# Performance work log

Hardware: AMD Instinct MI355X
Metric: run time of the kernel (lower is better)

The kernel has to match this reference:

```python
import jax, jax.numpy as jnp
import numpy as np

M, N, D = 100000, 64, 128  # points, channels, voxel grid side


def setup_inputs() -> dict:
    key = jax.random.key(0)
    k1, k2, k3, k4, k5 = jax.random.split(key, 5)
    rng = np.random.default_rng(0)
    # unique occupied voxels in a D^3 grid (Minkowski coords are unique)
    lin = rng.choice(D ** 3, size=M, replace=False)
    coords = np.stack(np.unravel_index(lin, (D, D, D)), axis=1).astype(np.int32)
    w_scale = 0.02  # ~1/sqrt(fan_in=27*N)
    return {
        "feats": jax.random.normal(k1, (M, N), dtype=jnp.float32),
        "W1": jax.random.normal(k2, (27, N, N), dtype=jnp.float32) * w_scale,
        "b1": jax.random.normal(k3, (N,), dtype=jnp.float32) * 0.01,
        "W2": jax.random.normal(k4, (27, N, N), dtype=jnp.float32) * w_scale,
        "b2": jax.random.normal(k5, (N,), dtype=jnp.float32) * 0.01,
        "coords": jnp.asarray(coords),
        "grid_size": D,
    }


def reference(feats, W1, b1, W2, b2, coords, grid_size):
    Dg = grid_size
    m = feats.shape[0]
    # dense hash: linear voxel id -> point index (-1 if empty)
    lin = (coords[:, 0].astype(jnp.int32) * Dg + coords[:, 1]) * Dg + coords[:, 2]
    lookup = jnp.full((Dg * Dg * Dg,), -1, dtype=jnp.int32).at[lin].set(
        jnp.arange(m, dtype=jnp.int32))
    offsets = jnp.array([[i, j, k] for i in (-1, 0, 1) for j in (-1, 0, 1)
                         for k in (-1, 0, 1)], dtype=jnp.int32)  # [27,3]

    def sparse_conv(x, W, b):
        # out[u] = b + sum_k W_k^T gather(x, u+off_k); scan over 27 offsets keeps
        # only one [M,N] gathered buffer live (memory-bound gather-GEMM-scatter)
        def step(acc, wk_off):
            W_k, off = wk_off
            nc = coords + off  # [M,3]
            inb = jnp.all((nc >= 0) & (nc < Dg), axis=1)
            nlin = (nc[:, 0] * Dg + nc[:, 1]) * Dg + nc[:, 2]
            nidx = lookup[jnp.where(inb, nlin, 0)]
            valid = inb & (nidx >= 0)
            g = jnp.where(valid[:, None], x[jnp.maximum(nidx, 0)], 0.0)  # [M,N]
            return acc + g @ W_k, None
        init = jnp.zeros_like(x) + b
        out, _ = jax.lax.scan(step, init, (W, offsets))
        return out

    h = jax.nn.relu(sparse_conv(feats, W1, b1))
    return jax.nn.relu(sparse_conv(h, W2, b2))
```

## Files before the change

### kernel.cpp

```cpp
#include <hip/hip_runtime.h>
#include <hip/hip_bf16.h>
#include <cstdint>
#include <cstddef>

typedef _Float16 half8 __attribute__((ext_vector_type(8)));
typedef float floatx16 __attribute__((ext_vector_type(16)));

#define DGRID 128
#define D3 (DGRID * DGRID * DGRID)
#define WSZ (2 * 27 * 4096)

struct __attribute__((aligned(4))) I3 { int a, b, c; };

__global__ void prep(const int* __restrict__ coords, const float* __restrict__ feats,
                     const float* __restrict__ W1, const float* __restrict__ W2,
                     int* __restrict__ lookup, _Float16* __restrict__ Whf,
                     _Float16* __restrict__ h0, _Float16* __restrict__ h, int M) {
    int tid = blockIdx.x * 256 + threadIdx.x;
    if (tid < WSZ) {
        int idx = tid;
        int j = idx & 7;
        int l = (idx >> 3) & 63;
        int f = (idx >> 9) & 7;
        int kL = idx >> 12;
        int k = kL % 27, L = kL / 27;
        int kk = f & 3, ct = f >> 2;
        int c = kk * 16 + (l >> 5) * 8 + j;
        int n = ct * 32 + (l & 31);
        const float* W = L ? W2 : W1;
        Whf[idx] = (_Float16)W[k * 4096 + c * 64 + n];
        return;
    }
    tid -= WSZ;
    if (tid < M) {
        int x = coords[3 * tid], y = coords[3 * tid + 1], z = coords[3 * tid + 2];
        lookup[(x * DGRID + y) * DGRID + z] = tid;
        return;
    }
    tid -= M;
    if (tid < 64) {
        h0[(size_t)M * 64 + tid] = (_Float16)0.f;
        h[(size_t)M * 64 + tid] = (_Float16)0.f;
        return;
    }
    tid -= 64;
    if (tid < M * 8) {
        const float4* src = (const float4*)feats + (size_t)tid * 2;
        float4 f0 = src[0], f1 = src[1];
        half8 v;
        v[0] = (_Float16)f0.x; v[1] = (_Float16)f0.y;
        v[2] = (_Float16)f0.z; v[3] = (_Float16)f0.w;
        v[4] = (_Float16)f1.x; v[5] = (_Float16)f1.y;
        v[6] = (_Float16)f1.z; v[7] = (_Float16)f1.w;
        ((half8*)h0)[tid] = v;
    }
}

template <bool FIRST, bool OUT_F16>
__global__ __launch_bounds__(64, 1) void spconv(const _Float16* __restrict__ x,
                                                const _Float16* __restrict__ Whf,
                                                const float* __restrict__ bias,
                                                const int* __restrict__ coords,
                                                const int* __restrict__ lookup,
                                                int* __restrict__ nbr,
                                                void* __restrict__ outp, int M) {
    __shared__ int nvs[27 * 128];
    const int lane = threadIdx.x;
    const int lrow = lane & 31;
    const int lhalf = lane >> 5;
    const int mw = blockIdx.x * 128;

#pragma unroll
    for (int half = 0; half < 2; ++half) {
        const int r = half * 64 + lane;
        const int row = mw + r;
        if constexpr (FIRST) {
            if (row < M) {
                int X = coords[3 * row], Y = coords[3 * row + 1], Z = coords[3 * row + 2];
                int zlo = Z - 1;
                if (zlo < 0) zlo = 0;
                if (zlo > DGRID - 3) zlo = DGRID - 3;
                const int zi = Z - zlo;
#pragma unroll
                for (int dx = -1; dx <= 1; ++dx)
#pragma unroll
                    for (int dy = -1; dy <= 1; ++dy) {
                        int nx = X + dx, ny = Y + dy;
                        int v0 = -1, v1 = -1, v2 = -1;
                        if (((unsigned)nx < DGRID) && ((unsigned)ny < DGRID)) {
                            I3 t = *(const I3*)(lookup + ((nx * DGRID + ny) * DGRID + zlo));
                            v0 = t.a; v1 = t.b; v2 = t.c;
                        }
#pragma unroll
                        for (int dz = -1; dz <= 1; ++dz) {
                            int zc = Z + dz;
                            int i = zi + dz;
                            int val = (i == 0) ? v0 : (i == 1) ? v1 : v2;
                            int nidx = M;
                            if (((unsigned)zc < DGRID) && ((unsigned)val < (unsigned)M))
                                nidx = val;
                            int k = (dx + 1) * 9 + (dy + 1) * 3 + (dz + 1);
                            nvs[k * 128 + r] = nidx;
                            nbr[(size_t)k * M + row] = nidx;
                        }
                    }
            } else {
#pragma unroll
                for (int k = 0; k < 27; ++k) nvs[k * 128 + r] = M;
            }
        } else {
            const int rc = row < M ? row : M - 1;
#pragma unroll
            for (int k = 0; k < 27; ++k) nvs[k * 128 + r] = nbr[(size_t)k * M + rc];
        }
    }
    __syncthreads();

    floatx16 acc[8];
#pragma unroll
    for (int i = 0; i < 8; ++i)
#pragma unroll
        for (int j = 0; j < 16; ++j) acc[i][j] = 0.0f;

    const half8* wb = (const half8*)Whf + lane;

    auto loadB = [&](half8* dst, int k) {
#pragma unroll
        for (int f = 0; f < 8; ++f) dst[f] = wb[(k * 8 + f) * 64];
    };
    auto loadA = [&](half8* dst, const int* nv) {
#pragma unroll
        for (int rt = 0; rt < 4; ++rt) {
            const half8* p = (const half8*)(x + (size_t)nv[rt] * 64 + lhalf * 8);
#pragma unroll
            for (int kk = 0; kk < 4; ++kk) dst[rt * 4 + kk] = p[kk * 2];
        }
    };

    int nvr[4][4];
#pragma unroll
    for (int j = 0; j < 3; ++j)
#pragma unroll
        for (int rt = 0; rt < 4; ++rt) nvr[j][rt] = nvs[j * 128 + rt * 32 + lrow];

    half8 Ar[3][16], Br[2][8];
    loadB(Br[0], 0);
    loadA(Ar[0], nvr[0]);
    loadA(Ar[1], nvr[1]);

#pragma unroll
    for (int i = 0; i < 27; ++i) {
        {
            int jn = i + 3;
            if (jn < 27) {
#pragma unroll
                for (int rt = 0; rt < 4; ++rt)
                    nvr[jn & 3][rt] = nvs[jn * 128 + rt * 32 + lrow];
            }
        }
        if (i + 1 < 27) loadB(Br[(i + 1) & 1], i + 1);
        {
            int ja = i + 2;
            if (ja < 27) loadA(Ar[ja % 3], nvr[ja & 3]);
        }
        __builtin_amdgcn_sched_barrier(0);
        half8* A = Ar[i % 3];
        half8* B = Br[i & 1];
#pragma unroll
        for (int kk = 0; kk < 4; ++kk)
#pragma unroll
            for (int rt = 0; rt < 4; ++rt)
#pragma unroll
                for (int ct = 0; ct < 2; ++ct)
                    acc[rt * 2 + ct] = __builtin_amdgcn_mfma_f32_32x32x16_f16(
                        A[rt * 4 + kk], B[ct * 4 + kk], acc[rt * 2 + ct], 0, 0, 0);
    }

    const float bv0 = bias[lrow], bv1 = bias[32 + lrow];
#pragma unroll
    for (int rt = 0; rt < 4; ++rt)
#pragma unroll
        for (int ct = 0; ct < 2; ++ct) {
            const float bb = ct ? bv1 : bv0;
#pragma unroll
            for (int reg = 0; reg < 16; ++reg) {
                int row = (reg & 3) + 8 * (reg >> 2) + 4 * lhalf;
                int g = mw + rt * 32 + row;
                if (g < M) {
                    float v = acc[rt * 2 + ct][reg] + bb;
                    v = v > 0.f ? v : 0.f;
                    size_t off = (size_t)g * 64 + ct * 32 + lrow;
                    if constexpr (OUT_F16)
                        ((_Float16*)outp)[off] = (_Float16)v;
                    else
                        ((float*)outp)[off] = v;
                }
            }
        }
}

extern "C" void kernel_launch(void* const* d_in, const int* in_sizes, int n_in,
                              void* d_out, int out_size, void* d_ws, size_t ws_size,
                              hipStream_t stream) {
    const float* feats = (const float*)d_in[0];
    const float* W1 = (const float*)d_in[1];
    const float* b1 = (const float*)d_in[2];
    const float* W2 = (const float*)d_in[3];
    const float* b2 = (const float*)d_in[4];
    const int* coords = (const int*)d_in[5];
    const int M = in_sizes[0] / 64;

    int* lookup = (int*)d_ws;
    int* nbr = lookup + (size_t)D3;
    _Float16* h = (_Float16*)(nbr + (size_t)27 * M);
    _Float16* h0 = h + (size_t)(M + 1) * 64;
    _Float16* Whf = h0 + (size_t)(M + 1) * 64;
    size_t need = (size_t)D3 * 4 + (size_t)27 * M * 4 +
                  2 * (size_t)(M + 1) * 64 * 2 + (size_t)WSZ * 2;
    if (ws_size < need) return;

    long long pt = (long long)WSZ + M + 64 + (long long)M * 8;
    prep<<<(int)((pt + 255) / 256), 256, 0, stream>>>(coords, feats, W1, W2, lookup, Whf,
                                                      h0, h, M);

    int cb = (M + 127) / 128;
    spconv<true, true><<<cb, 64, 0, stream>>>(h0, Whf, b1, coords, lookup, nbr,
                                              (void*)h, M);
    spconv<false, false><<<cb, 64, 0, stream>>>(h, Whf + (size_t)27 * 4096, b2, coords,
                                                lookup, nbr, d_out, M);
}
```

Before: 175.0 us.

## Split 128-row tile across four waves, one 32-row strip each

Each spconv block now runs 256 threads (four waves) instead of one wave. Each wave computes a 32-row strip of the 128-row tile, so per-thread accumulators and A-operand registers shrink by four. The neighbor-table fill is split across two thread halves. The intent is higher occupancy and more latency hiding for the gather loads. The cost is that every wave loads the full weight slice redundantly, which quadruples weight traffic per block.

After: 196.4 us. 12.2% more time.

```diff
diff --git a/kernel.cpp b/kernel.cpp
--- a/kernel.cpp
+++ b/kernel.cpp
@@ -57,23 +57,26 @@
 }
 
 template <bool FIRST, bool OUT_F16>
-__global__ __launch_bounds__(64, 1) void spconv(const _Float16* __restrict__ x,
-                                                const _Float16* __restrict__ Whf,
-                                                const float* __restrict__ bias,
-                                                const int* __restrict__ coords,
-                                                const int* __restrict__ lookup,
-                                                int* __restrict__ nbr,
-                                                void* __restrict__ outp, int M) {
+__global__ __launch_bounds__(256, 2) void spconv(const _Float16* __restrict__ x,
+                                                 const _Float16* __restrict__ Whf,
+                                                 const float* __restrict__ bias,
+                                                 const int* __restrict__ coords,
+                                                 const int* __restrict__ lookup,
+                                                 int* __restrict__ nbr,
+                                                 void* __restrict__ outp, int M) {
     __shared__ int nvs[27 * 128];
-    const int lane = threadIdx.x;
+    const int tid = threadIdx.x;
+    const int lane = tid & 63;
+    const int wid = tid >> 6;
     const int lrow = lane & 31;
     const int lhalf = lane >> 5;
     const int mw = blockIdx.x * 128;
-
-#pragma unroll
-    for (int half = 0; half < 2; ++half) {
-        const int r = half * 64 + lane;
-        const int row = mw + r;
+    const int wr = wid * 32;
+
+    {
+        const int rr = tid & 127;
+        const int kh = tid >> 7;
+        const int row = mw + rr;
         if constexpr (FIRST) {
             if (row < M) {
                 int X = coords[3 * row], Y = coords[3 * row + 1], Z = coords[3 * row + 2];
@@ -81,44 +84,46 @@
                 if (zlo < 0) zlo = 0;
                 if (zlo > DGRID - 3) zlo = DGRID - 3;
                 const int zi = Z - zlo;
-#pragma unroll
-                for (int dx = -1; dx <= 1; ++dx)
-#pragma unroll
-                    for (int dy = -1; dy <= 1; ++dy) {
-                        int nx = X + dx, ny = Y + dy;
-                        int v0 = -1, v1 = -1, v2 = -1;
-                        if (((unsigned)nx < DGRID) && ((unsigned)ny < DGRID)) {
-                            I3 t = *(const I3*)(lookup + ((nx * DGRID + ny) * DGRID + zlo));
-                            v0 = t.a; v1 = t.b; v2 = t.c;
-                        }
-#pragma unroll
-                        for (int dz = -1; dz <= 1; ++dz) {
-                            int zc = Z + dz;
-                            int i = zi + dz;
-                            int val = (i == 0) ? v0 : (i == 1) ? v1 : v2;
-                            int nidx = M;
-                            if (((unsigned)zc < DGRID) && ((unsigned)val < (unsigned)M))
-                                nidx = val;
-                            int k = (dx + 1) * 9 + (dy + 1) * 3 + (dz + 1);
-                            nvs[k * 128 + r] = nidx;
-                            nbr[(size_t)k * M + row] = nidx;
-                        }
+                const int p0 = kh ? 5 : 0, p1 = kh ? 9 : 5;
+#pragma unroll
+                for (int p = p0; p < p1; ++p) {
+                    int dx = p / 3 - 1, dy = p % 3 - 1;
+                    int nx = X + dx, ny = Y + dy;
+                    int v0 = -1, v1 = -1, v2 = -1;
+                    if (((unsigned)nx < DGRID) && ((unsigned)ny < DGRID)) {
+                        I3 t = *(const I3*)(lookup + ((nx * DGRID + ny) * DGRID + zlo));
+                        v0 = t.a; v1 = t.b; v2 = t.c;
                     }
+#pragma unroll
+                    for (int dz = -1; dz <= 1; ++dz) {
+                        int zc = Z + dz;
+                        int i = zi + dz;
+                        int val = (i == 0) ? v0 : (i == 1) ? v1 : v2;
+                        int nidx = M;
+                        if (((unsigned)zc < DGRID) && ((unsigned)val < (unsigned)M))
+                            nidx = val;
+                        int k = p * 3 + (dz + 1);
+                        nvs[k * 128 + rr] = nidx;
+                        nbr[(size_t)k * M + row] = nidx;
+                    }
+                }
             } else {
-#pragma unroll
-                for (int k = 0; k < 27; ++k) nvs[k * 128 + r] = M;
+                const int k0 = kh ? 15 : 0, k1 = kh ? 27 : 15;
+#pragma unroll
+                for (int k = k0; k < k1; ++k) nvs[k * 128 + rr] = M;
             }
         } else {
             const int rc = row < M ? row : M - 1;
-#pragma unroll
-            for (int k = 0; k < 27; ++k) nvs[k * 128 + r] = nbr[(size_t)k * M + rc];
+            const int k0 = kh ? 14 : 0, k1 = kh ? 27 : 14;
+#pragma unroll
+            for (int k = k0; k < k1; ++k) nvs[k * 128 + rr] = nbr[(size_t)k * M + rc];
         }
     }
     __syncthreads();
 
-    floatx16 acc[8];
-#pragma unroll
-    for (int i = 0; i < 8; ++i)
+    floatx16 acc[2];
+#pragma unroll
+    for (int i = 0; i < 2; ++i)
 #pragma unroll
         for (int j = 0; j < 16; ++j) acc[i][j] = 0.0f;
 
@@ -128,22 +133,17 @@
 #pragma unroll
         for (int f = 0; f < 8; ++f) dst[f] = wb[(k * 8 + f) * 64];
     };
-    auto loadA = [&](half8* dst, const int* nv) {
-#pragma unroll
-        for (int rt = 0; rt < 4; ++rt) {
-            const half8* p = (const half8*)(x + (size_t)nv[rt] * 64 + lhalf * 8);
-#pragma unroll
-            for (int kk = 0; kk < 4; ++kk) dst[rt * 4 + kk] = p[kk * 2];
-        }
+    auto loadA = [&](half8* dst, int nv) {
+        const half8* p = (const half8*)(x + (size_t)nv * 64 + lhalf * 8);
+#pragma unroll
+        for (int kk = 0; kk < 4; ++kk) dst[kk] = p[kk * 2];
     };
 
-    int nvr[4][4];
-#pragma unroll
-    for (int j = 0; j < 3; ++j)
-#pragma unroll
-        for (int rt = 0; rt < 4; ++rt) nvr[j][rt] = nvs[j * 128 + rt * 32 + lrow];
-
-    half8 Ar[3][16], Br[2][8];
+    int nvr[4];
+#pragma unroll
+    for (int j = 0; j < 3; ++j) nvr[j] = nvs[j * 128 + wr + lrow];
+
+    half8 Ar[3][4], Br[2][8];
     loadB(Br[0], 0);
     loadA(Ar[0], nvr[0]);
     loadA(Ar[1], nvr[1]);
@@ -152,11 +152,7 @@
     for (int i = 0; i < 27; ++i) {
         {
             int jn = i + 3;
-            if (jn < 27) {
-#pragma unroll
-                for (int rt = 0; rt < 4; ++rt)
-                    nvr[jn & 3][rt] = nvs[jn * 128 + rt * 32 + lrow];
-            }
+            if (jn < 27) nvr[jn & 3] = nvs[jn * 128 + wr + lrow];
         }
         if (i + 1 < 27) loadB(Br[(i + 1) & 1], i + 1);
         {
@@ -169,34 +165,30 @@
 #pragma unroll
         for (int kk = 0; kk < 4; ++kk)
 #pragma unroll
-            for (int rt = 0; rt < 4; ++rt)
-#pragma unroll
-                for (int ct = 0; ct < 2; ++ct)
-                    acc[rt * 2 + ct] = __builtin_amdgcn_mfma_f32_32x32x16_f16(
-                        A[rt * 4 + kk], B[ct * 4 + kk], acc[rt * 2 + ct], 0, 0, 0);
+            for (int ct = 0; ct < 2; ++ct)
+                acc[ct] = __builtin_amdgcn_mfma_f32_32x32x16_f16(
+                    A[kk], B[ct * 4 + kk], acc[ct], 0, 0, 0);
     }
 
     const float bv0 = bias[lrow], bv1 = bias[32 + lrow];
 #pragma unroll
-    for (int rt = 0; rt < 4; ++rt)
-#pragma unroll
-        for (int ct = 0; ct < 2; ++ct) {
-            const float bb = ct ? bv1 : bv0;
-#pragma unroll
-            for (int reg = 0; reg < 16; ++reg) {
-                int row = (reg & 3) + 8 * (reg >> 2) + 4 * lhalf;
-                int g = mw + rt * 32 + row;
-                if (g < M) {
-                    float v = acc[rt * 2 + ct][reg] + bb;
-                    v = v > 0.f ? v : 0.f;
-                    size_t off = (size_t)g * 64 + ct * 32 + lrow;
-                    if constexpr (OUT_F16)
-                        ((_Float16*)outp)[off] = (_Float16)v;
-                    else
-                        ((float*)outp)[off] = v;
-                }
+    for (int ct = 0; ct < 2; ++ct) {
+        const float bb = ct ? bv1 : bv0;
+#pragma unroll
+        for (int reg = 0; reg < 16; ++reg) {
+            int row = (reg & 3) + 8 * (reg >> 2) + 4 * lhalf;
+            int g = mw + wr + row;
+            if (g < M) {
+                float v = acc[ct][reg] + bb;
+                v = v > 0.f ? v : 0.f;
+                size_t off = (size_t)g * 64 + ct * 32 + lrow;
+                if constexpr (OUT_F16)
+                    ((_Float16*)outp)[off] = (_Float16)v;
+                else
+                    ((float*)outp)[off] = v;
             }
         }
+    }
 }
 
 extern "C" void kernel_launch(void* const* d_in, const int* in_sizes, int n_in,
@@ -224,8 +216,8 @@
                                                       h0, h, M);
 
     int cb = (M + 127) / 128;
-    spconv<true, true><<<cb, 64, 0, stream>>>(h0, Whf, b1, coords, lookup, nbr,
-                                              (void*)h, M);
-    spconv<false, false><<<cb, 64, 0, stream>>>(h, Whf + (size_t)27 * 4096, b2, coords,
-                                                lookup, nbr, d_out, M);
+    spconv<true, true><<<cb, 256, 0, stream>>>(h0, Whf, b1, coords, lookup, nbr,
+                                               (void*)h, M);
+    spconv<false, false><<<cb, 256, 0, stream>>>(h, Whf + (size_t)27 * 4096, b2, coords,
+                                                 lookup, nbr, d_out, M);
 }
```
